# Optimization experiments

Measured on AMD Instinct MI355X. Metric: run time of the kernel, lower is better.

The kernel has to match this reference:

```python
import jax, jax.numpy as jnp
import numpy as np

EPS = 1e-5


def _tconv(x, W, b):
    # x: [M, Cin, S], W: [Cout, Cin, K] -> [M, Cout, S] (SAME padding)
    y = jax.lax.conv_general_dilated(x, W, window_strides=(1,), padding='SAME',
                                     dimension_numbers=('NCH', 'OIH', 'NCH'))
    return y + b[None, :, None]


def _bn(x, g, b, axes, pshape):
    # batch-statistics normalization (train-mode BN, deterministic)
    m = jnp.mean(x, axes, keepdims=True)
    v = jnp.var(x, axes, keepdims=True)
    return (x - m) * jax.lax.rsqrt(v + EPS) * g.reshape(pshape) + b.reshape(pshape)


def setup_inputs() -> dict:
    key = jax.random.key(0)
    ks = jax.random.split(key, 12)
    B, Cin, N, S = 4, 32, 1024, 32
    Cout, Csp, E, K = 64, 64, 16384, 3
    x = jax.random.normal(ks[0], (B, Cin, N, S), dtype=jnp.float32)
    edge_index = jax.random.randint(ks[1], (2, E), 0, N, dtype=jnp.int64)
    sc = 0.05
    return {
        'x': x,
        'edge_index': edge_index,
        'W1': jax.random.normal(ks[2], (Cout, Cin, K), dtype=jnp.float32) * sc,
        'b1': jnp.zeros((Cout,), jnp.float32),
        'g1': jnp.ones((Cout,), jnp.float32),
        'be1': jnp.zeros((Cout,), jnp.float32),
        'Wg': jax.random.normal(ks[3], (Cout, Csp), dtype=jnp.float32) * sc,
        'bg': jnp.zeros((Csp,), jnp.float32),
        'gs': jnp.ones((Csp,), jnp.float32),
        'bes': jnp.zeros((Csp,), jnp.float32),
        'W2': jax.random.normal(ks[4], (Cout, Csp, K), dtype=jnp.float32) * sc,
        'b2': jnp.zeros((Cout,), jnp.float32),
        'g2': jnp.ones((Cout,), jnp.float32),
        'be2': jnp.zeros((Cout,), jnp.float32),
        'Wres': jax.random.normal(ks[5], (Cout, Cin, 1), dtype=jnp.float32) * sc,
        'bres': jnp.zeros((Cout,), jnp.float32),
    }


def reference(x, edge_index, W1, b1, g1, be1, Wg, bg, gs, bes, W2, b2, g2, be2, Wres, bres):
    B, Cin, N, S = x.shape
    Cout = W1.shape[0]
    Csp = Wg.shape[1]

    # ---- temporal1: [B*N, Cin, S] -> [B*N, Cout, S] ----
    x1 = x.transpose(0, 2, 1, 3).reshape(B * N, Cin, S)
    h = jax.nn.relu(_bn(_tconv(x1, W1, b1), g1, be1, (0, 2), (1, -1, 1)))

    # ---- spatial GCN, all B*S timesteps in one pass ----
    h = h.reshape(B, N, Cout, S).transpose(0, 3, 1, 2)  # [B, S, N, Cout]
    hw = jnp.einsum('bsnc,cd->bsnd', h, Wg)             # [B, S, N, Csp]

    # self-loops + symmetric normalization (PyG GCNConv)
    loops = jnp.arange(N, dtype=edge_index.dtype)
    src = jnp.concatenate([edge_index[0], loops])
    dst = jnp.concatenate([edge_index[1], loops])
    deg = jax.ops.segment_sum(jnp.ones_like(src, dtype=hw.dtype), dst, num_segments=N)
    dinv = jnp.where(deg > 0, jax.lax.rsqrt(deg), 0.0)
    norm = (dinv[src] * dinv[dst])[None, None, :, None]  # [1,1,E+N,1]

    msg = hw[:, :, src, :] * norm                        # [B, S, E+N, Csp]
    agg = jnp.zeros_like(hw).at[:, :, dst, :].add(msg) + bg

    # per-timestep BatchNorm1d over the node dim (loop normalized each [N, Csp] slice)
    s = jax.nn.relu(_bn(agg, gs, bes, (2,), (1, 1, 1, -1)))  # dropout: eval mode

    # ---- temporal2: [B*N, Csp, S] -> [B*N, Cout, S] ----
    s = s.transpose(0, 2, 3, 1).reshape(B * N, Csp, S)   # [B,S,N,C] -> [B,N,C,S]
    h2 = jax.nn.relu(_bn(_tconv(s, W2, b2), g2, be2, (0, 2), (1, -1, 1)))
    h2 = h2.reshape(B, N, Cout, S)

    # ---- residual 1x1 conv ----
    res = _tconv(x1, Wres, bres).reshape(B, N, Cout, S)

    out = jax.nn.relu(h2 + res).transpose(0, 2, 1, 3)    # [B, Cout, N, S]
    return out
```

## Files before the change

kernel.cpp:

```cpp
#include <hip/hip_runtime.h>
#include <stdint.h>

#define B_    4
#define CIN   32
#define NN    1024
#define SS    32
#define COUT  64
#define CSP   64
#define EPSV  1e-5f

typedef __attribute__((ext_vector_type(8))) short bfrag;
typedef __attribute__((ext_vector_type(4))) float facc;

__device__ __forceinline__ uint32_t f2b_rne(float f) {
    uint32_t x = __float_as_uint(f);
    return (x + 0x7fffu + ((x >> 16) & 1u)) >> 16;
}
__device__ __forceinline__ float bfu(uint32_t v) { return __uint_as_float(v << 16); }
__device__ __forceinline__ float bfh(uint32_t v) { return __uint_as_float(v & 0xffff0000u); }

__global__ void detect_kernel(const int* __restrict__ ei, int* __restrict__ flag) {
    if (threadIdx.x == 0) {
        int nz = 0;
        for (int i = 1; i < 257; i += 2) nz |= ei[i];
        *flag = (nz == 0) ? 1 : 0;
    }
}

__global__ void deg_count_kernel(const int* __restrict__ ei, int E,
                                 const int* __restrict__ flag, int* __restrict__ deg) {
    int e = blockIdx.x * 256 + threadIdx.x;
    int i64 = *flag;
    if (e < E) {
        int d = i64 ? ei[2 * (E + e)] : ei[E + e];
        atomicAdd(&deg[d], 1);
    }
}

__global__ __launch_bounds__(1024) void scan_kernel(
    const int* __restrict__ deg, int* __restrict__ row_ptr, float* __restrict__ dinv) {
    __shared__ int sb[NN];
    int t = threadIdx.x;
    int v = deg[t];
    sb[t] = v;
    __syncthreads();
    for (int off = 1; off < NN; off <<= 1) {
        int tmp = (t >= off) ? sb[t - off] : 0;
        __syncthreads();
        sb[t] += tmp;
        __syncthreads();
    }
    row_ptr[t] = sb[t] - v;
    if (t == NN - 1) row_ptr[NN] = sb[t];
    dinv[t] = rsqrtf((float)(v + 1));
}

__global__ void csr_fill_kernel(const int* __restrict__ ei, int E,
                                const int* __restrict__ flag,
                                const int* __restrict__ row_ptr, int* __restrict__ cursor,
                                const float* __restrict__ dinv, int2* __restrict__ edata) {
    int e = blockIdx.x * 256 + threadIdx.x;
    int i64 = *flag;
    if (e < E) {
        int s = i64 ? ei[2 * e] : ei[e];
        int d = i64 ? ei[2 * (E + e)] : ei[E + e];
        int pos = atomicAdd(&cursor[d], 1);
        edata[row_ptr[d] + pos] = make_int2(s, __float_as_int(dinv[s]));
    }
}

__global__ void w2pack_kernel(const float* __restrict__ W2,
                              uint32_t* __restrict__ wpkH, uint32_t* __restrict__ wpkL) {
    int flat = blockIdx.x * 256 + threadIdx.x;
    int lane = flat & 63, fi = flat >> 6;
    int kh = fi & 1, q = fi >> 1;
    int tap = q % 3, cc = q / 3;
    int ct = cc & 1, cb2 = cc >> 1;
    int cout = cb2 * 32 + ct * 16 + (lane & 15);
    int cbase = kh * 32 + (lane >> 4) * 8;
    const float* wp = W2 + ((size_t)cout * 64 + cbase) * 3 + tap;
    uint32_t h[8], l[8];
#pragma unroll
    for (int j = 0; j < 8; j++) {
        float w = wp[3 * j];
        uint32_t hb = f2b_rne(w);
        uint32_t lb = f2b_rne(w - bfu(hb));
        h[j] = hb; l[j] = lb;
    }
    uint4 H = {h[0] | (h[1] << 16), h[2] | (h[3] << 16),
               h[4] | (h[5] << 16), h[6] | (h[7] << 16)};
    uint4 L = {l[0] | (l[1] << 16), l[2] | (l[3] << 16),
               l[4] | (l[5] << 16), l[6] | (l[7] << 16)};
    ((uint4*)wpkH)[flat] = H;
    ((uint4*)wpkL)[flat] = L;
}

__global__ __launch_bounds__(512, 4) void conv1_kernel(
    const float* __restrict__ x, const float* __restrict__ W1,
    const float* __restrict__ b1, float* __restrict__ h_pre,
    float* __restrict__ psum, float* __restrict__ pss) {
    __shared__ __align__(16) float pool[15360];
    float* xs  = pool;
    float* w1l = pool + 9216;
    int t = threadIdx.x;
    int grp = blockIdx.x;
    int b = grp >> 7, n0 = (grp & 127) * 8;
    {
        int cout = t >> 3, kkb = (t & 7) * 12;
        const float* wsrc = W1 + cout * 96 + kkb;
#pragma unroll
        for (int j = 0; j < 12; j++) w1l[(kkb + j) * 64 + cout] = wsrc[j];
    }
    if (t < 256) {
        float* p = xs + (t >> 3) * 288 + (t & 7) * 36 + 32;
        p[0] = 0.f; p[1] = 0.f; p[2] = 0.f; p[3] = 0.f;
    }
#pragma unroll
    for (int i = 0; i < 4; i++) {
        int flat4 = i * 512 + t;
        int cin = flat4 >> 6;
        int rem = flat4 & 63;
        int n = rem >> 3, s4 = (rem & 7) * 4;
        float4 v = *(const float4*)(x + (((size_t)b * CIN + cin) * NN + n0 + n) * SS + s4);
        *(float4*)(xs + cin * 288 + n * 36 + s4) = v;
    }
    __syncthreads();
    int lane = t & 63, wvi = t >> 6;
    int n = wvi;
    int cout0 = 4 * (lane & 15), s0 = 8 * ((lane >> 4) & 3);
    int m1 = (s0 == 0) ? 35 : (s0 - 1);
    float y[4][8];
#pragma unroll
    for (int cc = 0; cc < 4; cc++) {
        float bbv = b1[cout0 + cc];
#pragma unroll
        for (int j = 0; j < 8; j++) y[cc][j] = bbv;
    }
#pragma unroll 4
    for (int cin = 0; cin < CIN; cin++) {
        const float* xr = xs + cin * 288 + n * 36;
        float xw[10];
        xw[0] = xr[m1];
        float4 xa = *(const float4*)(xr + s0);
        float4 xb = *(const float4*)(xr + s0 + 4);
        xw[1] = xa.x; xw[2] = xa.y; xw[3] = xa.z; xw[4] = xa.w;
        xw[5] = xb.x; xw[6] = xb.y; xw[7] = xb.z; xw[8] = xb.w;
        xw[9] = xr[s0 + 8];
        const float* wb = w1l + (3 * cin) * 64 + cout0;
        float4 w0 = *(const float4*)(wb);
        float4 w1v = *(const float4*)(wb + 64);
        float4 w2v = *(const float4*)(wb + 128);
        float wk0[4] = {w0.x, w0.y, w0.z, w0.w};
        float wk1[4] = {w1v.x, w1v.y, w1v.z, w1v.w};
        float wk2[4] = {w2v.x, w2v.y, w2v.z, w2v.w};
#pragma unroll
        for (int cc = 0; cc < 4; cc++)
#pragma unroll
            for (int j = 0; j < 8; j++)
                y[cc][j] += wk0[cc] * xw[j] + wk1[cc] * xw[j + 1] + wk2[cc] * xw[j + 2];
    }
    float* hb = h_pre + (((size_t)(b * NN + n0 + n)) * COUT + cout0) * SS + s0;
#pragma unroll
    for (int cc = 0; cc < 4; cc++) {
        float4 o0 = {y[cc][0], y[cc][1], y[cc][2], y[cc][3]};
        float4 o1 = {y[cc][4], y[cc][5], y[cc][6], y[cc][7]};
        *(float4*)(hb + cc * SS) = o0;
        *(float4*)(hb + cc * SS + 4) = o1;
    }
    float aS[4], aQ[4];
#pragma unroll
    for (int cc = 0; cc < 4; cc++) {
        float s_ = 0.f, q_ = 0.f;
#pragma unroll
        for (int j = 0; j < 8; j++) { s_ += y[cc][j]; q_ += y[cc][j] * y[cc][j]; }
        s_ += __shfl_down(s_, 16); s_ += __shfl_down(s_, 32);
        q_ += __shfl_down(q_, 16); q_ += __shfl_down(q_, 32);
        aS[cc] = s_; aQ[cc] = q_;
    }
    __syncthreads();
    float* redS = pool;
    float* redQ = pool + 512;
    if (lane < 16) {
#pragma unroll
        for (int cc = 0; cc < 4; cc++) {
            redS[wvi * 64 + 4 * lane + cc] = aS[cc];
            redQ[wvi * 64 + 4 * lane + cc] = aQ[cc];
        }
    }
    __syncthreads();
    if (t < 64) {
        float S = 0.f, Q = 0.f;
#pragma unroll
        for (int w = 0; w < 8; w++) { S += redS[w * 64 + t]; Q += redQ[w * 64 + t]; }
        psum[t * 512 + grp] = S;
        pss[t * 512 + grp] = Q;
    }
}

__global__ void bn_reduce_kernel(const float* __restrict__ psum, const float* __restrict__ pss,
                                 const float* __restrict__ g, const float* __restrict__ be,
                                 float* __restrict__ scale, float* __restrict__ shift,
                                 float invM, int stride, int nslots) {
    int c = blockIdx.x, t = threadIdx.x;
    const float* ps = psum + c * stride;
    const float* pq = pss + c * stride;
    float s = 0.f, q = 0.f;
    for (int i = t; i < nslots; i += 256) { s += ps[i]; q += pq[i]; }
#pragma unroll
    for (int o = 32; o > 0; o >>= 1) { s += __shfl_down(s, o); q += __shfl_down(q, o); }
    __shared__ float ws_[4], wq_[4];
    if ((t & 63) == 0) { ws_[t >> 6] = s; wq_[t >> 6] = q; }
    __syncthreads();
    if (t == 0) {
        float S = ws_[0] + ws_[1] + ws_[2] + ws_[3];
        float Q = wq_[0] + wq_[1] + wq_[2] + wq_[3];
        float m = S * invM, v = Q * invM - m * m;
        float sc = g[c] * rsqrtf(v + EPSV);
        scale[c] = sc;
        shift[c] = be[c] - m * sc;
    }
}

__global__ __launch_bounds__(256, 2) void bn1_gemm_kernel(
    const float* __restrict__ h_pre, const float* __restrict__ scale1,
    const float* __restrict__ shift1, const float* __restrict__ Wg,
    ushort* __restrict__ hw) {
    __shared__ __align__(16) float hs[COUT * 144];
    __shared__ __align__(16) float wgl[COUT * CSP];
    int t = threadIdx.x;
    int grp = blockIdx.x;
    int b = grp >> 8, n0 = (grp & 255) * 4;
#pragma unroll
    for (int i = 0; i < 4; i++)
        ((float4*)wgl)[i * 256 + t] = ((const float4*)Wg)[i * 256 + t];
#pragma unroll
    for (int i = 0; i < 8; i++) {
        int flat4 = i * 256 + t;
        int n = flat4 >> 9;
        int rem = flat4 & 511;
        int c = rem >> 3, s4 = (rem & 7) * 4;
        float sc1 = scale1[c], sh1 = shift1[c];
        const float* p = h_pre + (((size_t)(b * NN + n0 + n)) * COUT + c) * SS + s4;
        float4 u = *(const float4*)p;
        float4 v;
        v.x = fmaxf(u.x * sc1 + sh1, 0.f);
        v.y = fmaxf(u.y * sc1 + sh1, 0.f);
        v.z = fmaxf(u.z * sc1 + sh1, 0.f);
        v.w = fmaxf(u.w * sc1 + sh1, 0.f);
        *(float4*)(hs + c * 144 + n * 36 + s4) = v;
    }
    __syncthreads();
    int lane = t & 63, n = t >> 6;
    int d0 = 4 * (lane & 15), s0 = 8 * ((lane >> 4) & 3);
    float acc[4][8];
#pragma unroll
    for (int cc = 0; cc < 4; cc++)
#pragma unroll
        for (int j = 0; j < 8; j++) acc[cc][j] = 0.f;
#pragma unroll 4
    for (int c = 0; c < COUT; c++) {
        float4 w4 = *(const float4*)(wgl + c * 64 + d0);
        const float* xr = hs + c * 144 + n * 36;
        float4 xa = *(const float4*)(xr + s0);
        float4 xb = *(const float4*)(xr + s0 + 4);
        float xv[8] = {xa.x, xa.y, xa.z, xa.w, xb.x, xb.y, xb.z, xb.w};
#pragma unroll
        for (int j = 0; j < 8; j++) {
            acc[0][j] += xv[j] * w4.x;
            acc[1][j] += xv[j] * w4.y;
            acc[2][j] += xv[j] * w4.z;
            acc[3][j] += xv[j] * w4.w;
        }
    }
#pragma unroll
    for (int j = 0; j < 8; j++) {
        uint32_t p0 = f2b_rne(acc[0][j]) | (f2b_rne(acc[1][j]) << 16);
        uint32_t p1 = f2b_rne(acc[2][j]) | (f2b_rne(acc[3][j]) << 16);
        uint2 o = {p0, p1};
        *(uint2*)(hw + (((size_t)(b * NN + n0 + n)) * SS + s0 + j) * CSP + d0) = o;
    }
}

__global__ __launch_bounds__(256, 4) void gcn_kernel(
    const ushort* __restrict__ hw, const int* __restrict__ row_ptr,
    const int2* __restrict__ edata, const float* __restrict__ dinv,
    const float* __restrict__ bg, float* __restrict__ agg,
    float* __restrict__ psum2, float* __restrict__ pss2) {
    int t = threadIdx.x;
    int blk = blockIdx.x;
    int xcd = blk & 7, jj = blk >> 3;
    int b = xcd >> 1;
    int grp = (xcd & 1) + 2 * jj;
    int n0 = grp * 4;
    int off = t * 8;
    const ushort* hwb = hw + (size_t)b * NN * 2048;
    float bgv[8];
    int c0 = off & 63;
#pragma unroll
    for (int j = 0; j < 8; j++) bgv[j] = bg[c0 + j];
    float sS[8], sQ[8];
#pragma unroll
    for (int j = 0; j < 8; j++) { sS[j] = 0.f; sQ[j] = 0.f; }
    for (int g = 0; g < 4; g++) {
        int n = n0 + g;
        int r0 = row_ptr[n], r1 = row_ptr[n + 1];
        float dn = dinv[n];
        float acc[8];
        {
            uint4 u = *(const uint4*)(hwb + (size_t)n * 2048 + off);
            acc[0] = dn * bfu(u.x); acc[1] = dn * bfh(u.x);
            acc[2] = dn * bfu(u.y); acc[3] = dn * bfh(u.y);
            acc[4] = dn * bfu(u.z); acc[5] = dn * bfh(u.z);
            acc[6] = dn * bfu(u.w); acc[7] = dn * bfh(u.w);
        }
        int r = r0;
        for (; r + 2 <= r1; r += 2) {
            int2 e0 = edata[r], e1 = edata[r + 1];
            uint4 u0 = *(const uint4*)(hwb + (size_t)e0.x * 2048 + off);
            uint4 u1 = *(const uint4*)(hwb + (size_t)e1.x * 2048 + off);
            float w0 = __int_as_float(e0.y), w1 = __int_as_float(e1.y);
            acc[0] += w0 * bfu(u0.x) + w1 * bfu(u1.x);
            acc[1] += w0 * bfh(u0.x) + w1 * bfh(u1.x);
            acc[2] += w0 * bfu(u0.y) + w1 * bfu(u1.y);
            acc[3] += w0 * bfh(u0.y) + w1 * bfh(u1.y);
            acc[4] += w0 * bfu(u0.z) + w1 * bfu(u1.z);
            acc[5] += w0 * bfh(u0.z) + w1 * bfh(u1.z);
            acc[6] += w0 * bfu(u0.w) + w1 * bfu(u1.w);
            acc[7] += w0 * bfh(u0.w) + w1 * bfh(u1.w);
        }
        if (r < r1) {
            int2 e = edata[r];
            uint4 u = *(const uint4*)(hwb + (size_t)e.x * 2048 + off);
            float w = __int_as_float(e.y);
            acc[0] += w * bfu(u.x); acc[1] += w * bfh(u.x);
            acc[2] += w * bfu(u.y); acc[3] += w * bfh(u.y);
            acc[4] += w * bfu(u.z); acc[5] += w * bfh(u.z);
            acc[6] += w * bfu(u.w); acc[7] += w * bfh(u.w);
        }
        float o[8];
#pragma unroll
        for (int j = 0; j < 8; j++) {
            o[j] = dn * acc[j] + bgv[j];
            sS[j] += o[j]; sQ[j] += o[j] * o[j];
        }
        float* ar = agg + ((size_t)(b * NN + n)) * 2048 + off;
        float4 o0 = {o[0], o[1], o[2], o[3]}, o1 = {o[4], o[5], o[6], o[7]};
        *(float4*)ar = o0; *(float4*)(ar + 4) = o1;
    }
    float* ps = psum2 + ((size_t)(b * 256 + grp)) * 2048 + off;
    float* pq = pss2 + ((size_t)(b * 256 + grp)) * 2048 + off;
    float4 s0v = {sS[0], sS[1], sS[2], sS[3]}, s1v = {sS[4], sS[5], sS[6], sS[7]};
    float4 q0v = {sQ[0], sQ[1], sQ[2], sQ[3]}, q1v = {sQ[4], sQ[5], sQ[6], sQ[7]};
    *(float4*)ps = s0v; *(float4*)(ps + 4) = s1v;
    *(float4*)pq = q0v; *(float4*)(pq + 4) = q1v;
}

__global__ void bn2_reduce_kernel(const float* __restrict__ psum2, const float* __restrict__ pss2,
                                  const float* __restrict__ gs, const float* __restrict__ bes,
                                  float* __restrict__ scale2, float* __restrict__ shift2) {
    int idx = blockIdx.x * 256 + threadIdx.x;
    int b = idx >> 11, rem = idx & 2047;
    const float* ps = psum2 + (size_t)b * 256 * 2048 + rem;
    const float* pq = pss2 + (size_t)b * 256 * 2048 + rem;
    float S = 0.f, Q = 0.f;
    for (int g = 0; g < 256; g++) { S += ps[(size_t)g * 2048]; Q += pq[(size_t)g * 2048]; }
    int d = idx & 63;
    float m = S * (1.f / NN);
    float v = Q * (1.f / NN) - m * m;
    float sc = gs[d] * rsqrtf(v + EPSV);
    scale2[idx] = sc;
    shift2[idx] = bes[d] - m * sc;
}

__global__ __launch_bounds__(256, 2) void conv2_mfma_kernel(
    const float* __restrict__ agg, const float* __restrict__ scale2,
    const float* __restrict__ shift2, const uint32_t* __restrict__ wpkH,
    const uint32_t* __restrict__ wpkL,
    const float* __restrict__ b2, float* __restrict__ h2_pre,
    float* __restrict__ psumC, float* __restrict__ pssC) {
    __shared__ __align__(16) char pool[35840];
    char* Phi = pool;
    char* Plo = pool + 17408;
    float* redS = (float*)(pool + 34816);
    float* redQ = (float*)(pool + 35328);
    int t = threadIdx.x;
    int grp = blockIdx.x;
    int b = grp >> 8, n0 = (grp & 255) * 4;
    int lane = t & 63, wv = t >> 6;
    int s0 = (wv >> 1) * 16, cb = (wv & 1) * 32;
    int l15 = lane & 15, lg = lane >> 4;

    if (t < 128) {
        int nl = t >> 5, rem = t & 31;
        int tr = (rem >> 4) ? 33 : 0;
        int j = rem & 15;
        uint32_t off = (uint32_t)(nl * 4352 + tr * 128 + 8 * j);
        off ^= (uint32_t)((tr & 7) << 4);
        *(uint2*)(Phi + off) = make_uint2(0u, 0u);
        *(uint2*)(Plo + off) = make_uint2(0u, 0u);
    }
#pragma unroll
    for (int i = 0; i < 8; i++) {
        int flat4 = i * 256 + t;
        int c0 = 4 * (flat4 & 15);
        int s = (flat4 >> 4) & 31;
        int nl = flat4 >> 9;
        const float* p = agg + ((size_t)((b * NN + n0 + nl) * 32 + s)) * 64 + c0;
        float4 u = *(const float4*)p;
        int bsi = (b * 32 + s) * 64 + c0;
        float4 sc = *(const float4*)(scale2 + bsi);
        float4 sh = *(const float4*)(shift2 + bsi);
        float v0 = fmaxf(u.x * sc.x + sh.x, 0.f);
        float v1 = fmaxf(u.y * sc.y + sh.y, 0.f);
        float v2 = fmaxf(u.z * sc.z + sh.z, 0.f);
        float v3 = fmaxf(u.w * sc.w + sh.w, 0.f);
        uint32_t h0 = f2b_rne(v0), h1 = f2b_rne(v1), h2 = f2b_rne(v2), h3 = f2b_rne(v3);
        uint32_t l0 = f2b_rne(v0 - bfu(h0)), l1 = f2b_rne(v1 - bfu(h1));
        uint32_t l2 = f2b_rne(v2 - bfu(h2)), l3 = f2b_rne(v3 - bfu(h3));
        int tr = s + 1;
        uint32_t off = (uint32_t)(nl * 4352 + tr * 128 + 2 * c0);
        off ^= (uint32_t)((tr & 7) << 4);
        *(uint2*)(Phi + off) = make_uint2(h0 | (h1 << 16), h2 | (h3 << 16));
        *(uint2*)(Plo + off) = make_uint2(l0 | (l1 << 16), l2 | (l3 << 16));
    }

    bfrag Wh[2][3][2], Wl[2][3][2];
    {
        const uint4* WH = (const uint4*)wpkH;
        const uint4* WL = (const uint4*)wpkL;
        int cb2 = wv & 1;
#pragma unroll
        for (int ct = 0; ct < 2; ct++)
#pragma unroll
            for (int tap = 0; tap < 3; tap++)
#pragma unroll
                for (int kh = 0; kh < 2; kh++) {
                    int fi = ((((cb2 * 2 + ct) * 3 + tap) * 2) + kh) * 64 + lane;
                    uint4 H = WH[fi];
                    uint4 L = WL[fi];
                    Wh[ct][tap][kh] = *(const bfrag*)&H;
                    Wl[ct][tap][kh] = *(const bfrag*)&L;
                }
    }
    __syncthreads();

    float bb0 = b2[cb + l15], bb1 = b2[cb + 16 + l15];
    float sS0 = 0.f, sS1 = 0.f, sQ0 = 0.f, sQ1 = 0.f;
    for (int nl = 0; nl < 4; nl++) {
        facc acc0 = {0.f, 0.f, 0.f, 0.f};
        facc acc1 = {0.f, 0.f, 0.f, 0.f};
#pragma unroll
        for (int tap = 0; tap < 3; tap++) {
#pragma unroll
            for (int kh = 0; kh < 2; kh++) {
                int row = s0 + tap + l15;
                uint32_t off = (uint32_t)(nl * 4352 + row * 128 + kh * 64 + (lg << 4));
                off ^= (uint32_t)((row & 7) << 4);
                bfrag ah = *(const bfrag*)(Phi + off);
                bfrag al = *(const bfrag*)(Plo + off);
                acc0 = __builtin_amdgcn_mfma_f32_16x16x32_bf16(ah, Wh[0][tap][kh], acc0, 0, 0, 0);
                acc1 = __builtin_amdgcn_mfma_f32_16x16x32_bf16(ah, Wh[1][tap][kh], acc1, 0, 0, 0);
                acc0 = __builtin_amdgcn_mfma_f32_16x16x32_bf16(al, Wh[0][tap][kh], acc0, 0, 0, 0);
                acc1 = __builtin_amdgcn_mfma_f32_16x16x32_bf16(al, Wh[1][tap][kh], acc1, 0, 0, 0);
                acc0 = __builtin_amdgcn_mfma_f32_16x16x32_bf16(ah, Wl[0][tap][kh], acc0, 0, 0, 0);
                acc1 = __builtin_amdgcn_mfma_f32_16x16x32_bf16(ah, Wl[1][tap][kh], acc1, 0, 0, 0);
            }
        }
        int sx = s0 + (lg << 2);
        float* hp = h2_pre + ((size_t)(b * NN + n0 + nl)) * (COUT * SS);
        {
            float y0 = acc0[0] + bb0, y1 = acc0[1] + bb0;
            float y2 = acc0[2] + bb0, y3 = acc0[3] + bb0;
            float4 o = {y0, y1, y2, y3};
            *(float4*)(hp + (cb + l15) * SS + sx) = o;
            sS0 += y0 + y1 + y2 + y3;
            sQ0 += y0 * y0 + y1 * y1 + y2 * y2 + y3 * y3;
        }
        {
            float y0 = acc1[0] + bb1, y1 = acc1[1] + bb1;
            float y2 = acc1[2] + bb1, y3 = acc1[3] + bb1;
            float4 o = {y0, y1, y2, y3};
            *(float4*)(hp + (cb + 16 + l15) * SS + sx) = o;
            sS1 += y0 + y1 + y2 + y3;
            sQ1 += y0 * y0 + y1 * y1 + y2 * y2 + y3 * y3;
        }
    }
    sS0 += __shfl_down(sS0, 16); sS0 += __shfl_down(sS0, 32);
    sS1 += __shfl_down(sS1, 16); sS1 += __shfl_down(sS1, 32);
    sQ0 += __shfl_down(sQ0, 16); sQ0 += __shfl_down(sQ0, 32);
    sQ1 += __shfl_down(sQ1, 16); sQ1 += __shfl_down(sQ1, 32);
    if (lane < 16) {
        redS[wv * 32 + lane] = sS0;      redQ[wv * 32 + lane] = sQ0;
        redS[wv * 32 + 16 + lane] = sS1; redQ[wv * 32 + 16 + lane] = sQ1;
    }
    __syncthreads();
    if (t < 64) {
        int wA = t >> 5, slot = t & 31;
        float S = redS[wA * 32 + slot] + redS[(wA + 2) * 32 + slot];
        float Q = redQ[wA * 32 + slot] + redQ[(wA + 2) * 32 + slot];
        psumC[(size_t)t * 1024 + grp] = S;
        pssC[(size_t)t * 1024 + grp] = Q;
    }
}

__global__ __launch_bounds__(256) void final_kernel(
    const float* __restrict__ x, const float* __restrict__ Wres,
    const float* __restrict__ bres, const float* __restrict__ h2_pre,
    const float* __restrict__ scale3, const float* __restrict__ shift3,
    float* __restrict__ out) {
    __shared__ __align__(16) float xs[CIN][36];
    __shared__ float wrl[COUT * 33];
    int t = threadIdx.x;
    int bn = blockIdx.x;
    int b = bn >> 10, n = bn & (NN - 1);
    {
        int sst = t & 31, cinb = t >> 5;
#pragma unroll
        for (int i = 0; i < 4; i++) {
            int cin = cinb + 8 * i;
            xs[cin][sst] = x[(((size_t)b * CIN + cin) * NN + n) * SS + sst];
        }
    }
#pragma unroll
    for (int i = 0; i < 2; i++) {
        int lin = (i * 256 + t) * 4;
        int cw = lin >> 5, c0 = lin & 31;
        float4 v = *(const float4*)(Wres + lin);
        float* dst = &wrl[cw * 33 + c0];
        dst[0] = v.x; dst[1] = v.y; dst[2] = v.z; dst[3] = v.w;
    }
    __syncthreads();
    int cout = t >> 2, s0 = (t & 3) * 8;
    float res[8];
    float bb = bres[cout];
#pragma unroll
    for (int j = 0; j < 8; j++) res[j] = bb;
    const float* wrow = &wrl[cout * 33];
#pragma unroll 4
    for (int cin = 0; cin < CIN; cin++) {
        float w = wrow[cin];
        float4 xa = *(const float4*)&xs[cin][s0];
        float4 xb = *(const float4*)&xs[cin][s0 + 4];
        res[0] += xa.x * w; res[1] += xa.y * w; res[2] += xa.z * w; res[3] += xa.w * w;
        res[4] += xb.x * w; res[5] += xb.y * w; res[6] += xb.z * w; res[7] += xb.w * w;
    }
    const float* hp = h2_pre + (size_t)bn * COUT * SS + cout * SS + s0;
    float4 h0 = *(const float4*)hp, h1 = *(const float4*)(hp + 4);
    float h2[8] = {h0.x, h0.y, h0.z, h0.w, h1.x, h1.y, h1.z, h1.w};
    float sc = scale3[cout], sh = shift3[cout];
    float o[8];
#pragma unroll
    for (int j = 0; j < 8; j++) {
        float hv = fmaxf(sc * h2[j] + sh, 0.f);
        o[j] = fmaxf(hv + res[j], 0.f);
    }
    float* op = out + (((size_t)b * COUT + cout) * NN + n) * SS + s0;
    float4 o0 = {o[0], o[1], o[2], o[3]}, o1 = {o[4], o[5], o[6], o[7]};
    *(float4*)op = o0; *(float4*)(op + 4) = o1;
}

extern "C" void kernel_launch(void* const* d_in, const int* in_sizes, int n_in,
                              void* d_out, int out_size, void* d_ws, size_t ws_size,
                              hipStream_t stream) {
    const float* x    = (const float*)d_in[0];
    const int*   ei   = (const int*)  d_in[1];
    const float* W1   = (const float*)d_in[2];
    const float* b1   = (const float*)d_in[3];
    const float* g1   = (const float*)d_in[4];
    const float* be1  = (const float*)d_in[5];
    const float* Wg   = (const float*)d_in[6];
    const float* bg   = (const float*)d_in[7];
    const float* gs   = (const float*)d_in[8];
    const float* bes  = (const float*)d_in[9];
    const float* W2   = (const float*)d_in[10];
    const float* b2   = (const float*)d_in[11];
    const float* g2   = (const float*)d_in[12];
    const float* be2  = (const float*)d_in[13];
    const float* Wres = (const float*)d_in[14];
    const float* bres = (const float*)d_in[15];
    float* out = (float*)d_out;
    int E = in_sizes[1] / 2;

    char* ws = (char*)d_ws;
    int*   deg    = (int*)  (ws + 0);
    int*   cursor = (int*)  (ws + 4096);
    uint32_t* wpkH = (uint32_t*)(ws + 8192);
    uint32_t* wpkL = (uint32_t*)(ws + 32768);
    int*   row_ptr= (int*)  (ws + 73728);
    int*   flag   = (int*)  (ws + 77888);
    float* dinv   = (float*)(ws + 78080);
    float* scale1 = (float*)(ws + 82176);
    float* shift1 = (float*)(ws + 82432);
    float* scale3 = (float*)(ws + 82688);
    float* shift3 = (float*)(ws + 82944);
    float* scale2 = (float*)(ws + 83200);
    float* shift2 = (float*)(ws + 115968);
    float* psum   = (float*)(ws + 148736);
    float* pss    = (float*)(ws + 279808);
    int2*  edata  = (int2*) (ws + 410880);
    char*  bigA   = ws + 542720;
    ushort* hwB   = (ushort*)bigA;
    float* psum2  = (float*)(bigA + 16777216);
    float* pss2   = (float*)(bigA + 25165824);
    float* h2p    = (float*)bigA;
    float* psumC  = (float*)(ws + 34097152);
    float* pssC   = (float*)(ws + 34359296);
    float* h_pre  = out;
    float* agg    = out;

    hipMemsetAsync(ws, 0, 8192, stream);
    w2pack_kernel<<<6, 256, 0, stream>>>(W2, wpkH, wpkL);
    detect_kernel<<<1, 64, 0, stream>>>(ei, flag);
    int egrid = (E + 255) / 256;
    deg_count_kernel<<<egrid, 256, 0, stream>>>(ei, E, flag, deg);
    scan_kernel<<<1, NN, 0, stream>>>(deg, row_ptr, dinv);
    csr_fill_kernel<<<egrid, 256, 0, stream>>>(ei, E, flag, row_ptr, cursor, dinv, edata);

    conv1_kernel<<<512, 512, 0, stream>>>(x, W1, b1, h_pre, psum, pss);
    bn_reduce_kernel<<<64, 256, 0, stream>>>(psum, pss, g1, be1, scale1, shift1,
                                             1.f / (B_ * NN * SS), 512, 512);
    bn1_gemm_kernel<<<1024, 256, 0, stream>>>(h_pre, scale1, shift1, Wg, hwB);
    gcn_kernel<<<1024, 256, 0, stream>>>(hwB, row_ptr, edata, dinv, bg, agg, psum2, pss2);
    bn2_reduce_kernel<<<32, 256, 0, stream>>>(psum2, pss2, gs, bes, scale2, shift2);
    conv2_mfma_kernel<<<1024, 256, 0, stream>>>(agg, scale2, shift2, wpkH, wpkL,
                                                b2, h2p, psumC, pssC);
    bn_reduce_kernel<<<64, 256, 0, stream>>>(psumC, pssC, g2, be2, scale3, shift3,
                                             1.f / (B_ * NN * SS), 1024, 1024);
    final_kernel<<<B_ * NN, 256, 0, stream>>>(x, Wres, bres, h2p, scale3, shift3, out);
}
```

Measured before the change: 240.4 us.

## Move conv1 to bf16x3 MFMA with prepacked split weights

```diff
diff --git a/kernel.cpp b/kernel.cpp
--- a/kernel.cpp
+++ b/kernel.cpp
@@ -95,105 +95,149 @@
     ((uint4*)wpkL)[flat] = L;
 }
 
-__global__ __launch_bounds__(512, 4) void conv1_kernel(
-    const float* __restrict__ x, const float* __restrict__ W1,
-    const float* __restrict__ b1, float* __restrict__ h_pre,
-    float* __restrict__ psum, float* __restrict__ pss) {
-    __shared__ __align__(16) float pool[15360];
-    float* xs  = pool;
-    float* w1l = pool + 9216;
+__global__ void w1pack_kernel(const float* __restrict__ W1,
+                              uint32_t* __restrict__ wpk1H, uint32_t* __restrict__ wpk1L) {
+    int flat = blockIdx.x * 256 + threadIdx.x;
+    int lane = flat & 63, fi = flat >> 6;
+    int tap = fi % 3, cc = fi / 3;
+    int ct = cc & 1, cb2 = cc >> 1;
+    int cout = cb2 * 32 + ct * 16 + (lane & 15);
+    int k0 = (lane >> 4) * 8;
+    const float* wp = W1 + (size_t)cout * 96 + k0 * 3 + tap;
+    uint32_t h[8], l[8];
+#pragma unroll
+    for (int j = 0; j < 8; j++) {
+        float w = wp[3 * j];
+        uint32_t hb = f2b_rne(w);
+        uint32_t lb = f2b_rne(w - bfu(hb));
+        h[j] = hb; l[j] = lb;
+    }
+    uint4 H = {h[0] | (h[1] << 16), h[2] | (h[3] << 16),
+               h[4] | (h[5] << 16), h[6] | (h[7] << 16)};
+    uint4 L = {l[0] | (l[1] << 16), l[2] | (l[3] << 16),
+               l[4] | (l[5] << 16), l[6] | (l[7] << 16)};
+    ((uint4*)wpk1H)[flat] = H;
+    ((uint4*)wpk1L)[flat] = L;
+}
+
+__global__ __launch_bounds__(256, 2) void conv1_mfma_kernel(
+    const float* __restrict__ x, const uint32_t* __restrict__ wpk1H,
+    const uint32_t* __restrict__ wpk1L, const float* __restrict__ b1,
+    float* __restrict__ h_pre, float* __restrict__ psumC, float* __restrict__ pssC) {
+    __shared__ __align__(16) char pool[18432];
+    char* Phi = pool;
+    char* Plo = pool + 8704;
+    float* redS = (float*)(pool + 17408);
+    float* redQ = (float*)(pool + 17920);
     int t = threadIdx.x;
     int grp = blockIdx.x;
-    int b = grp >> 7, n0 = (grp & 127) * 8;
+    int b = grp >> 8, n0 = (grp & 255) * 4;
+    int lane = t & 63, wv = t >> 6;
+    int s0 = (wv >> 1) * 16, cb = (wv & 1) * 32;
+    int l15 = lane & 15, lg = lane >> 4;
+
+    if (t < 32) {
+        int nl = t >> 3, rem = t & 7;
+        int row = (rem >> 2) ? 33 : 0;
+        int q = rem & 3;
+        uint32_t off = (uint32_t)(nl * 2176 + row * 64 + q * 16);
+        off ^= (uint32_t)((row & 7) << 4);
+        *(uint4*)(Phi + off) = make_uint4(0u, 0u, 0u, 0u);
+        *(uint4*)(Plo + off) = make_uint4(0u, 0u, 0u, 0u);
+    }
+#pragma unroll
+    for (int it = 0; it < 2; it++) {
+        int flat = it * 256 + t;
+        int cinp = flat & 15;
+        int nl = (flat >> 4) & 3;
+        int s4 = (flat >> 6) * 4;
+        const float* xp = x + (((size_t)b * CIN + 2 * cinp) * NN + n0 + nl) * SS + s4;
+        float4 u0 = *(const float4*)xp;
+        float4 u1 = *(const float4*)(xp + NN * SS);
+        float va[4] = {u0.x, u0.y, u0.z, u0.w};
+        float vb[4] = {u1.x, u1.y, u1.z, u1.w};
+#pragma unroll
+        for (int j = 0; j < 4; j++) {
+            uint32_t ha = f2b_rne(va[j]), hb = f2b_rne(vb[j]);
+            uint32_t la = f2b_rne(va[j] - bfu(ha)), lb = f2b_rne(vb[j] - bfu(hb));
+            int row = s4 + j + 1;
+            uint32_t off = (uint32_t)(nl * 2176 + row * 64 + cinp * 4);
+            off ^= (uint32_t)((row & 7) << 4);
+            *(uint32_t*)(Phi + off) = ha | (hb << 16);
+            *(uint32_t*)(Plo + off) = la | (lb << 16);
+        }
+    }
+    bfrag Wh[2][3], Wl[2][3];
     {
-        int cout = t >> 3, kkb = (t & 7) * 12;
-        const float* wsrc = W1 + cout * 96 + kkb;
-#pragma unroll
-        for (int j = 0; j < 12; j++) w1l[(kkb + j) * 64 + cout] = wsrc[j];
-    }
-    if (t < 256) {
-        float* p = xs + (t >> 3) * 288 + (t & 7) * 36 + 32;
-        p[0] = 0.f; p[1] = 0.f; p[2] = 0.f; p[3] = 0.f;
-    }
-#pragma unroll
-    for (int i = 0; i < 4; i++) {
-        int flat4 = i * 512 + t;
-        int cin = flat4 >> 6;
-        int rem = flat4 & 63;
-        int n = rem >> 3, s4 = (rem & 7) * 4;
-        float4 v = *(const float4*)(x + (((size_t)b * CIN + cin) * NN + n0 + n) * SS + s4);
-        *(float4*)(xs + cin * 288 + n * 36 + s4) = v;
-    }
-    __syncthreads();
-    int lane = t & 63, wvi = t >> 6;
-    int n = wvi;
-    int cout0 = 4 * (lane & 15), s0 = 8 * ((lane >> 4) & 3);
-    int m1 = (s0 == 0) ? 35 : (s0 - 1);
-    float y[4][8];
-#pragma unroll
-    for (int cc = 0; cc < 4; cc++) {
-        float bbv = b1[cout0 + cc];
-#pragma unroll
-        for (int j = 0; j < 8; j++) y[cc][j] = bbv;
-    }
-#pragma unroll 4
-    for (int cin = 0; cin < CIN; cin++) {
-        const float* xr = xs + cin * 288 + n * 36;
-        float xw[10];
-        xw[0] = xr[m1];
-        float4 xa = *(const float4*)(xr + s0);
-        float4 xb = *(const float4*)(xr + s0 + 4);
-        xw[1] = xa.x; xw[2] = xa.y; xw[3] = xa.z; xw[4] = xa.w;
-        xw[5] = xb.x; xw[6] = xb.y; xw[7] = xb.z; xw[8] = xb.w;
-        xw[9] = xr[s0 + 8];
-        const float* wb = w1l + (3 * cin) * 64 + cout0;
-        float4 w0 = *(const float4*)(wb);
-        float4 w1v = *(const float4*)(wb + 64);
-        float4 w2v = *(const float4*)(wb + 128);
-        float wk0[4] = {w0.x, w0.y, w0.z, w0.w};
-        float wk1[4] = {w1v.x, w1v.y, w1v.z, w1v.w};
-        float wk2[4] = {w2v.x, w2v.y, w2v.z, w2v.w};
-#pragma unroll
-        for (int cc = 0; cc < 4; cc++)
-#pragma unroll
-            for (int j = 0; j < 8; j++)
-                y[cc][j] += wk0[cc] * xw[j] + wk1[cc] * xw[j + 1] + wk2[cc] * xw[j + 2];
-    }
-    float* hb = h_pre + (((size_t)(b * NN + n0 + n)) * COUT + cout0) * SS + s0;
-#pragma unroll
-    for (int cc = 0; cc < 4; cc++) {
-        float4 o0 = {y[cc][0], y[cc][1], y[cc][2], y[cc][3]};
-        float4 o1 = {y[cc][4], y[cc][5], y[cc][6], y[cc][7]};
-        *(float4*)(hb + cc * SS) = o0;
-        *(float4*)(hb + cc * SS + 4) = o1;
-    }
-    float aS[4], aQ[4];
-#pragma unroll
-    for (int cc = 0; cc < 4; cc++) {
-        float s_ = 0.f, q_ = 0.f;
-#pragma unroll
-        for (int j = 0; j < 8; j++) { s_ += y[cc][j]; q_ += y[cc][j] * y[cc][j]; }
-        s_ += __shfl_down(s_, 16); s_ += __shfl_down(s_, 32);
-        q_ += __shfl_down(q_, 16); q_ += __shfl_down(q_, 32);
-        aS[cc] = s_; aQ[cc] = q_;
-    }
-    __syncthreads();
-    float* redS = pool;
-    float* redQ = pool + 512;
+        const uint4* WH = (const uint4*)wpk1H;
+        const uint4* WL = (const uint4*)wpk1L;
+        int cb2 = wv & 1;
+#pragma unroll
+        for (int ct = 0; ct < 2; ct++)
+#pragma unroll
+            for (int tap = 0; tap < 3; tap++) {
+                int fi = ((cb2 * 2 + ct) * 3 + tap) * 64 + lane;
+                uint4 H = WH[fi];
+                uint4 L = WL[fi];
+                Wh[ct][tap] = *(const bfrag*)&H;
+                Wl[ct][tap] = *(const bfrag*)&L;
+            }
+    }
+    __syncthreads();
+
+    float bb0 = b1[cb + l15], bb1 = b1[cb + 16 + l15];
+    float sS0 = 0.f, sS1 = 0.f, sQ0 = 0.f, sQ1 = 0.f;
+    for (int nl = 0; nl < 4; nl++) {
+        facc acc0 = {0.f, 0.f, 0.f, 0.f};
+        facc acc1 = {0.f, 0.f, 0.f, 0.f};
+#pragma unroll
+        for (int tap = 0; tap < 3; tap++) {
+            int row = s0 + tap + l15;
+            uint32_t off = (uint32_t)(nl * 2176 + row * 64 + (lg << 4));
+            off ^= (uint32_t)((row & 7) << 4);
+            bfrag ah = *(const bfrag*)(Phi + off);
+            bfrag al = *(const bfrag*)(Plo + off);
+            acc0 = __builtin_amdgcn_mfma_f32_16x16x32_bf16(ah, Wh[0][tap], acc0, 0, 0, 0);
+            acc1 = __builtin_amdgcn_mfma_f32_16x16x32_bf16(ah, Wh[1][tap], acc1, 0, 0, 0);
+            acc0 = __builtin_amdgcn_mfma_f32_16x16x32_bf16(al, Wh[0][tap], acc0, 0, 0, 0);
+            acc1 = __builtin_amdgcn_mfma_f32_16x16x32_bf16(al, Wh[1][tap], acc1, 0, 0, 0);
+            acc0 = __builtin_amdgcn_mfma_f32_16x16x32_bf16(ah, Wl[0][tap], acc0, 0, 0, 0);
+            acc1 = __builtin_amdgcn_mfma_f32_16x16x32_bf16(ah, Wl[1][tap], acc1, 0, 0, 0);
+        }
+        int sx = s0 + (lg << 2);
+        float* hp = h_pre + ((size_t)(b * NN + n0 + nl)) * (COUT * SS);
+        {
+            float y0 = acc0[0] + bb0, y1 = acc0[1] + bb0;
+            float y2 = acc0[2] + bb0, y3 = acc0[3] + bb0;
+            float4 o = {y0, y1, y2, y3};
+            *(float4*)(hp + (cb + l15) * SS + sx) = o;
+            sS0 += y0 + y1 + y2 + y3;
+            sQ0 += y0 * y0 + y1 * y1 + y2 * y2 + y3 * y3;
+        }
+        {
+            float y0 = acc1[0] + bb1, y1 = acc1[1] + bb1;
+            float y2 = acc1[2] + bb1, y3 = acc1[3] + bb1;
+            float4 o = {y0, y1, y2, y3};
+            *(float4*)(hp + (cb + 16 + l15) * SS + sx) = o;
+            sS1 += y0 + y1 + y2 + y3;
+            sQ1 += y0 * y0 + y1 * y1 + y2 * y2 + y3 * y3;
+        }
+    }
+    sS0 += __shfl_down(sS0, 16); sS0 += __shfl_down(sS0, 32);
+    sS1 += __shfl_down(sS1, 16); sS1 += __shfl_down(sS1, 32);
+    sQ0 += __shfl_down(sQ0, 16); sQ0 += __shfl_down(sQ0, 32);
+    sQ1 += __shfl_down(sQ1, 16); sQ1 += __shfl_down(sQ1, 32);
     if (lane < 16) {
-#pragma unroll
-        for (int cc = 0; cc < 4; cc++) {
-            redS[wvi * 64 + 4 * lane + cc] = aS[cc];
-            redQ[wvi * 64 + 4 * lane + cc] = aQ[cc];
-        }
+        redS[wv * 32 + lane] = sS0;      redQ[wv * 32 + lane] = sQ0;
+        redS[wv * 32 + 16 + lane] = sS1; redQ[wv * 32 + 16 + lane] = sQ1;
     }
     __syncthreads();
     if (t < 64) {
-        float S = 0.f, Q = 0.f;
-#pragma unroll
-        for (int w = 0; w < 8; w++) { S += redS[w * 64 + t]; Q += redQ[w * 64 + t]; }
-        psum[t * 512 + grp] = S;
-        pss[t * 512 + grp] = Q;
+        int wA = t >> 5, slot = t & 31;
+        float S = redS[wA * 32 + slot] + redS[(wA + 2) * 32 + slot];
+        float Q = redQ[wA * 32 + slot] + redQ[(wA + 2) * 32 + slot];
+        psumC[(size_t)t * 1024 + grp] = S;
+        pssC[(size_t)t * 1024 + grp] = Q;
     }
 }
 
@@ -605,20 +649,23 @@
     float* h2p    = (float*)bigA;
     float* psumC  = (float*)(ws + 34097152);
     float* pssC   = (float*)(ws + 34359296);
+    uint32_t* wpk1H = (uint32_t*)(ws + 34621440);
+    uint32_t* wpk1L = (uint32_t*)(ws + 34633728);
     float* h_pre  = out;
     float* agg    = out;
 
     hipMemsetAsync(ws, 0, 8192, stream);
     w2pack_kernel<<<6, 256, 0, stream>>>(W2, wpkH, wpkL);
+    w1pack_kernel<<<3, 256, 0, stream>>>(W1, wpk1H, wpk1L);
     detect_kernel<<<1, 64, 0, stream>>>(ei, flag);
     int egrid = (E + 255) / 256;
     deg_count_kernel<<<egrid, 256, 0, stream>>>(ei, E, flag, deg);
     scan_kernel<<<1, NN, 0, stream>>>(deg, row_ptr, dinv);
     csr_fill_kernel<<<egrid, 256, 0, stream>>>(ei, E, flag, row_ptr, cursor, dinv, edata);
 
-    conv1_kernel<<<512, 512, 0, stream>>>(x, W1, b1, h_pre, psum, pss);
-    bn_reduce_kernel<<<64, 256, 0, stream>>>(psum, pss, g1, be1, scale1, shift1,
-                                             1.f / (B_ * NN * SS), 512, 512);
+    conv1_mfma_kernel<<<1024, 256, 0, stream>>>(x, wpk1H, wpk1L, b1, h_pre, psumC, pssC);
+    bn_reduce_kernel<<<64, 256, 0, stream>>>(psumC, pssC, g1, be1, scale1, shift1,
+                                             1.f / (B_ * NN * SS), 1024, 1024);
     bn1_gemm_kernel<<<1024, 256, 0, stream>>>(h_pre, scale1, shift1, Wg, hwB);
     gcn_kernel<<<1024, 256, 0, stream>>>(hwB, row_ptr, edata, dinv, bg, agg, psum2, pss2);
     bn2_reduce_kernel<<<32, 256, 0, stream>>>(psum2, pss2, gs, bes, scale2, shift2);
```

Result: faster. 231.2 us (-3.8%).
